# Performance work log

Hardware: AMD Instinct MI355X
Metric: run time of the kernel (lower is better)

## Reference

```python
import jax, jax.numpy as jnp
import numpy as np

B, N, F = 2, 1024, 128
H1, H2 = 64, 32


def setup_inputs() -> dict:
    key = jax.random.key(0)
    ks = jax.random.split(key, 8)
    x = jax.random.normal(ks[0], (B, N, F), dtype=jnp.float32)
    adj = jax.random.uniform(ks[1], (B, N, N), dtype=jnp.float32)
    mask = jnp.ones((B, N), dtype=bool)
    # torch.nn.Linear default init: U(-1/sqrt(fan_in), 1/sqrt(fan_in))
    s1 = 1.0 / np.sqrt(2 * F)
    s2 = 1.0 / np.sqrt(H1)
    s3 = 1.0 / np.sqrt(H2)
    W1 = jax.random.uniform(ks[2], (2 * F, H1), jnp.float32, -s1, s1)
    b1 = jax.random.uniform(ks[3], (H1,), jnp.float32, -s1, s1)
    W2 = jax.random.uniform(ks[4], (H1, H2), jnp.float32, -s2, s2)
    b2 = jax.random.uniform(ks[5], (H2,), jnp.float32, -s2, s2)
    W3 = jax.random.uniform(ks[6], (H2, 1), jnp.float32, -s3, s3)
    b3 = jax.random.uniform(ks[7], (1,), jnp.float32, -s3, s3)
    return {"x": x, "adj": adj, "mask": mask,
            "W1": W1, "b1": b1, "W2": W2, "b2": b2, "W3": W3, "b3": b3}


def reference(x, adj, mask, W1, b1, W2, b2, W3, b3):
    # Original: edge_pairwise[b,i,j] = concat(x[b,j], x[b,i]) -> MLP -> [B,N,N]
    # Faithful fused form: split W1 rows into the half applied to x_j and the
    # half applied to x_i; first Linear = x@Wj broadcast over i + x@Wi broadcast
    # over j + b1 (identical math, avoids the [B,N,N,2F] concat intermediate).
    f = x.shape[-1]
    Wj, Wi = W1[:f], W1[f:]
    pj = x @ Wj  # [B,N,H1], contribution of x[b,j]
    pi = x @ Wi  # [B,N,H1], contribution of x[b,i]
    h = jax.nn.relu(pj[:, None, :, :] + pi[:, :, None, :] + b1)  # [B,N,N,H1]
    h = jax.nn.relu(h @ W2 + b2)  # [B,N,N,H2]
    out = (h @ W3 + b3)[..., 0]   # [B,N,N]
    return out
```

## Files before the change

### kernel.cpp

```cpp
#include <hip/hip_runtime.h>

#define BB 2
#define NN 1024
#define FF 128
#define H1 64
#define H2 32
#define XPAD 136
#define PAD 72

typedef __attribute__((ext_vector_type(4))) _Float16 half4;
typedef __attribute__((ext_vector_type(8))) _Float16 half8;
typedef __attribute__((ext_vector_type(16))) float f32x16;
typedef __attribute__((ext_vector_type(2))) float f32x2;

__device__ inline half8 addrelu8(half8 a, half8 b) {
    half8 s = a + b;
    const half8 z = {};
    return __builtin_elementwise_max(s, z);
}

__global__ __launch_bounds__(512, 2) void fused_kernel(
    const float* __restrict__ x, const float* __restrict__ W1,
    const float* __restrict__ b1, const float* __restrict__ W2,
    const float* __restrict__ b2, const float* __restrict__ W3,
    const float* __restrict__ b3, float* __restrict__ out)
{
    __shared__ __align__(16) _Float16 xlds[128][XPAD];
    __shared__ __align__(16) _Float16 plds[64][PAD];
    __shared__ __align__(16) _Float16 pjlds[64][PAD];

    const int tid  = threadIdx.x;
    const int lane = tid & 63;
    const int wv   = tid >> 6;
    const int bid  = blockIdx.x;

    const int b   = bid >> 8;
    const int rem = bid & 255;
    const int i0  = (rem >> 4) * 64;
    const int j0  = (rem & 15) * 64;
    const int jn  = lane & 31;
    const int hi  = lane >> 5;
    const int m   = jn;

    {
        const int xb_i = b * NN + i0, xb_j = b * NN + j0 - 64;
        #pragma unroll
        for (int it = 0; it < 8; ++it) {
            const int idx = tid + it * 512;
            const int row = idx >> 5, c4 = (idx & 31) * 4;
            const int gr  = (row < 64 ? xb_i : xb_j) + row;
            const float4 v = *(const float4*)(x + (size_t)gr * FF + c4);
            half4 hv = {(_Float16)v.x, (_Float16)v.y,
                        (_Float16)v.z, (_Float16)v.w};
            *(half4*)&xlds[row][c4] = hv;
        }
    }
    __syncthreads();

    {
        const int xrow0 = ((wv & 2) ? 32 : 0) + ((wv & 4) ? 64 : 0);
        const int htile = wv & 1;
        const int koff  = (wv & 4) ? 0 : FF;
        _Float16* dstbase = (wv & 4) ? &pjlds[xrow0 - 64][0] : &plds[xrow0][0];
        const float* bias = (wv & 4) ? nullptr : b1;

        f32x16 acc = {};
        #pragma unroll
        for (int ks = 0; ks < 8; ++ks) {
            const int k0 = ks * 16 + hi * 8;
            half8 af;
            const float* wb = W1 + (size_t)(koff + k0) * H1 + htile * 32 + m;
            #pragma unroll
            for (int e = 0; e < 8; ++e)
                af[e] = (_Float16)wb[(size_t)e * H1];
            const half8 bf = *(const half8*)&xlds[xrow0 + m][k0];
            acc = __builtin_amdgcn_mfma_f32_32x32x16_f16(af, bf, acc, 0, 0, 0);
        }
        _Float16* drow = dstbase + (size_t)m * PAD;
        #pragma unroll
        for (int q = 0; q < 4; ++q) {
            half4 hv;
            #pragma unroll
            for (int jj = 0; jj < 4; ++jj) {
                const int r  = q * 4 + jj;
                const int hg = htile * 32 + 8 * q + 4 * hi + jj;
                float v = acc[r];
                if (bias) v += bias[hg];
                hv[jj] = (_Float16)v;
            }
            *(half4*)(drow + htile * 32 + 8 * q + 4 * hi) = hv;
        }
    }

    half8 wa[4];
    #pragma unroll
    for (int c4 = 0; c4 < 4; ++c4)
        #pragma unroll
        for (int e = 0; e < 8; ++e)
            wa[c4][e] = (_Float16)W2[(16 * c4 + hi * 8 + e) * H2 + jn];

    f32x16 ci;
    #pragma unroll
    for (int r = 0; r < 16; ++r) {
        const int row = (r & 3) + 8 * (r >> 2) + 4 * hi;
        ci[r] = b2[row];
    }
    f32x2 w32[8];
    #pragma unroll
    for (int q = 0; q < 8; ++q) {
        const int row = ((2 * q) & 3) + 8 * (q >> 1) + 4 * hi;
        w32[q] = (f32x2){W3[row], W3[row + 1]};
    }
    const float b3v = b3[0];

    __syncthreads();

    const int rowgrp = wv >> 1;
    const int jhalf  = wv & 1;

    const _Float16* pr = &pjlds[jhalf * 32 + jn][hi * 8];
    const half8 qj0 = *(const half8*)(pr);
    const half8 qj1 = *(const half8*)(pr + 16);
    const half8 qj2 = *(const half8*)(pr + 32);
    const half8 qj3 = *(const half8*)(pr + 48);

    auto epi = [&](const f32x16& dd) -> float {
        const f32x2 z2 = {0.f, 0.f};
        f32x2 s[4] = {z2, z2, z2, z2};
        #pragma unroll
        for (int q = 0; q < 8; ++q) {
            f32x2 dp = {dd[2 * q], dd[2 * q + 1]};
            dp = __builtin_elementwise_max(dp, z2);
            s[q & 3] = __builtin_elementwise_fma(dp, w32[q], s[q & 3]);
        }
        const f32x2 t01 = s[0] + s[1];
        const f32x2 t23 = s[2] + s[3];
        const f32x2 tt  = t01 + t23;
        float p = tt[0] + tt[1];
        p += __shfl_xor(p, 32);
        return p;
    };

    const _Float16* irbase = &plds[rowgrp * 16][hi * 8];
    float* obase = out + (size_t)(b * NN + i0 + rowgrp * 16) * NN
                       + j0 + jhalf * 32 + jn;

    half8 e0 = addrelu8(qj0, *(const half8*)(irbase));
    half8 e1 = addrelu8(qj1, *(const half8*)(irbase + 16));
    half8 e2 = addrelu8(qj2, *(const half8*)(irbase + 32));
    half8 e3 = addrelu8(qj3, *(const half8*)(irbase + 48));
    f32x16 dP;
    dP = __builtin_amdgcn_mfma_f32_32x32x16_f16(wa[0], e0, ci, 0, 0, 0);
    dP = __builtin_amdgcn_mfma_f32_32x32x16_f16(wa[1], e1, dP, 0, 0, 0);
    dP = __builtin_amdgcn_mfma_f32_32x32x16_f16(wa[2], e2, dP, 0, 0, 0);
    dP = __builtin_amdgcn_mfma_f32_32x32x16_f16(wa[3], e3, dP, 0, 0, 0);
    {
        const _Float16* ir = irbase + PAD;
        e0 = addrelu8(qj0, *(const half8*)(ir));
        e1 = addrelu8(qj1, *(const half8*)(ir + 16));
        e2 = addrelu8(qj2, *(const half8*)(ir + 32));
        e3 = addrelu8(qj3, *(const half8*)(ir + 48));
    }
    float pe = 0.f;

    #pragma unroll 2
    for (int t = 1; t < 16; ++t) {
        const int tn = (t < 15) ? t + 1 : 15;
        const _Float16* ir = irbase + tn * PAD;
        const half8 m0 = *(const half8*)(ir);
        const half8 m1 = *(const half8*)(ir + 16);
        const half8 m2 = *(const half8*)(ir + 32);
        const half8 m3 = *(const half8*)(ir + 48);
        f32x16 d;
        d = __builtin_amdgcn_mfma_f32_32x32x16_f16(wa[0], e0, ci, 0, 0, 0);
        d = __builtin_amdgcn_mfma_f32_32x32x16_f16(wa[1], e1, d,  0, 0, 0);
        d = __builtin_amdgcn_mfma_f32_32x32x16_f16(wa[2], e2, d,  0, 0, 0);
        d = __builtin_amdgcn_mfma_f32_32x32x16_f16(wa[3], e3, d,  0, 0, 0);
        const float p = epi(dP);
        if ((t - 1) & 1) {
            const float v = hi ? p : pe;
            obase[(size_t)(t - 2 + hi) * NN] = v + b3v;
        } else {
            pe = p;
        }
        e0 = addrelu8(qj0, m0);
        e1 = addrelu8(qj1, m1);
        e2 = addrelu8(qj2, m2);
        e3 = addrelu8(qj3, m3);
        dP = d;
    }
    {
        const float p = epi(dP);
        const float v = hi ? p : pe;
        obase[(size_t)(14 + hi) * NN] = v + b3v;
    }
}

extern "C" void kernel_launch(void* const* d_in, const int* in_sizes, int n_in,
                              void* d_out, int out_size, void* d_ws, size_t ws_size,
                              hipStream_t stream) {
    const float* x  = (const float*)d_in[0];
    const float* W1 = (const float*)d_in[3];
    const float* b1 = (const float*)d_in[4];
    const float* W2 = (const float*)d_in[5];
    const float* b2 = (const float*)d_in[6];
    const float* W3 = (const float*)d_in[7];
    const float* b3 = (const float*)d_in[8];
    float* out = (float*)d_out;

    fused_kernel<<<BB * NN * NN / (64 * 64), 512, 0, stream>>>(
        x, W1, b1, W2, b2, W3, b3, out);
}
```

Before: 22.95 us.

## Give each wave 8 rows over both j-halves with two interleaved MFMA chains

Each wave now handles 8 i-rows across all 64 j columns instead of 16 rows over one 32-column half. Every LDS row read of pi is reused for two independent MFMA accumulation chains (j-halves A and B), which halves the LDS reads per output. It also replaces the software-pipelined prefetch loop with a simple rolled loop. The two interleaved chains are meant to hide MFMA dependency latency. In exchange, register pressure rises from holding two sets of pj fragments and two accumulators, and the explicit load prefetch is lost.

```diff
diff --git a/kernel.cpp b/kernel.cpp
--- a/kernel.cpp
+++ b/kernel.cpp
@@ -115,14 +115,16 @@
 
     __syncthreads();
 
-    const int rowgrp = wv >> 1;
-    const int jhalf  = wv & 1;
-
-    const _Float16* pr = &pjlds[jhalf * 32 + jn][hi * 8];
-    const half8 qj0 = *(const half8*)(pr);
-    const half8 qj1 = *(const half8*)(pr + 16);
-    const half8 qj2 = *(const half8*)(pr + 32);
-    const half8 qj3 = *(const half8*)(pr + 48);
+    const _Float16* prA = &pjlds[jn][hi * 8];
+    const _Float16* prB = &pjlds[32 + jn][hi * 8];
+    const half8 qjA0 = *(const half8*)(prA);
+    const half8 qjA1 = *(const half8*)(prA + 16);
+    const half8 qjA2 = *(const half8*)(prA + 32);
+    const half8 qjA3 = *(const half8*)(prA + 48);
+    const half8 qjB0 = *(const half8*)(prB);
+    const half8 qjB1 = *(const half8*)(prB + 16);
+    const half8 qjB2 = *(const half8*)(prB + 32);
+    const half8 qjB3 = *(const half8*)(prB + 48);
 
     auto epi = [&](const f32x16& dd) -> float {
         const f32x2 z2 = {0.f, 0.f};
@@ -141,58 +143,37 @@
         return p;
     };
 
-    const _Float16* irbase = &plds[rowgrp * 16][hi * 8];
-    float* obase = out + (size_t)(b * NN + i0 + rowgrp * 16) * NN
-                       + j0 + jhalf * 32 + jn;
+    const _Float16* irbase = &plds[wv * 8][hi * 8];
+    float* obase = out + (size_t)(b * NN + i0 + wv * 8) * NN
+                       + j0 + hi * 32 + jn;
 
-    half8 e0 = addrelu8(qj0, *(const half8*)(irbase));
-    half8 e1 = addrelu8(qj1, *(const half8*)(irbase + 16));
-    half8 e2 = addrelu8(qj2, *(const half8*)(irbase + 32));
-    half8 e3 = addrelu8(qj3, *(const half8*)(irbase + 48));
-    f32x16 dP;
-    dP = __builtin_amdgcn_mfma_f32_32x32x16_f16(wa[0], e0, ci, 0, 0, 0);
-    dP = __builtin_amdgcn_mfma_f32_32x32x16_f16(wa[1], e1, dP, 0, 0, 0);
-    dP = __builtin_amdgcn_mfma_f32_32x32x16_f16(wa[2], e2, dP, 0, 0, 0);
-    dP = __builtin_amdgcn_mfma_f32_32x32x16_f16(wa[3], e3, dP, 0, 0, 0);
-    {
-        const _Float16* ir = irbase + PAD;
-        e0 = addrelu8(qj0, *(const half8*)(ir));
-        e1 = addrelu8(qj1, *(const half8*)(ir + 16));
-        e2 = addrelu8(qj2, *(const half8*)(ir + 32));
-        e3 = addrelu8(qj3, *(const half8*)(ir + 48));
-    }
-    float pe = 0.f;
-
-    #pragma unroll 2
-    for (int t = 1; t < 16; ++t) {
-        const int tn = (t < 15) ? t + 1 : 15;
-        const _Float16* ir = irbase + tn * PAD;
-        const half8 m0 = *(const half8*)(ir);
-        const half8 m1 = *(const half8*)(ir + 16);
-        const half8 m2 = *(const half8*)(ir + 32);
-        const half8 m3 = *(const half8*)(ir + 48);
-        f32x16 d;
-        d = __builtin_amdgcn_mfma_f32_32x32x16_f16(wa[0], e0, ci, 0, 0, 0);
-        d = __builtin_amdgcn_mfma_f32_32x32x16_f16(wa[1], e1, d,  0, 0, 0);
-        d = __builtin_amdgcn_mfma_f32_32x32x16_f16(wa[2], e2, d,  0, 0, 0);
-        d = __builtin_amdgcn_mfma_f32_32x32x16_f16(wa[3], e3, d,  0, 0, 0);
-        const float p = epi(dP);
-        if ((t - 1) & 1) {
-            const float v = hi ? p : pe;
-            obase[(size_t)(t - 2 + hi) * NN] = v + b3v;
-        } else {
-            pe = p;
-        }
-        e0 = addrelu8(qj0, m0);
-        e1 = addrelu8(qj1, m1);
-        e2 = addrelu8(qj2, m2);
-        e3 = addrelu8(qj3, m3);
-        dP = d;
-    }
-    {
-        const float p = epi(dP);
-        const float v = hi ? p : pe;
-        obase[(size_t)(14 + hi) * NN] = v + b3v;
+    #pragma unroll 1
+    for (int t = 0; t < 8; ++t) {
+        const _Float16* ir = irbase + t * PAD;
+        const half8 r0 = *(const half8*)(ir);
+        const half8 r1 = *(const half8*)(ir + 16);
+        const half8 r2 = *(const half8*)(ir + 32);
+        const half8 r3 = *(const half8*)(ir + 48);
+        const half8 a0 = addrelu8(qjA0, r0);
+        const half8 a1 = addrelu8(qjA1, r1);
+        const half8 a2 = addrelu8(qjA2, r2);
+        const half8 a3 = addrelu8(qjA3, r3);
+        const half8 g0 = addrelu8(qjB0, r0);
+        const half8 g1 = addrelu8(qjB1, r1);
+        const half8 g2 = addrelu8(qjB2, r2);
+        const half8 g3 = addrelu8(qjB3, r3);
+        f32x16 dA, dB;
+        dA = __builtin_amdgcn_mfma_f32_32x32x16_f16(wa[0], a0, ci, 0, 0, 0);
+        dB = __builtin_amdgcn_mfma_f32_32x32x16_f16(wa[0], g0, ci, 0, 0, 0);
+        dA = __builtin_amdgcn_mfma_f32_32x32x16_f16(wa[1], a1, dA, 0, 0, 0);
+        dB = __builtin_amdgcn_mfma_f32_32x32x16_f16(wa[1], g1, dB, 0, 0, 0);
+        dA = __builtin_amdgcn_mfma_f32_32x32x16_f16(wa[2], a2, dA, 0, 0, 0);
+        dB = __builtin_amdgcn_mfma_f32_32x32x16_f16(wa[2], g2, dB, 0, 0, 0);
+        dA = __builtin_amdgcn_mfma_f32_32x32x16_f16(wa[3], a3, dA, 0, 0, 0);
+        dB = __builtin_amdgcn_mfma_f32_32x32x16_f16(wa[3], g3, dB, 0, 0, 0);
+        const float pA = epi(dA);
+        const float pB = epi(dB);
+        obase[(size_t)t * NN] = (hi ? pB : pA) + b3v;
     }
 }
 
```

After: 24.84 us. 8.3% more time.
